# Optimization experiments

Measured on AMD Instinct MI355X. Metric: run time of the kernel, lower is better.

The kernel has to match this reference:

```python
import jax, jax.numpy as jnp
import numpy as np

N_NODES = 50000


def _gcn_norm(edge_index, num_nodes):
    # Add self-loops (PyG GCNConv default) and compute symmetric norm.
    loops = jnp.arange(num_nodes, dtype=edge_index.dtype)
    src = jnp.concatenate([edge_index[0], loops])
    dst = jnp.concatenate([edge_index[1], loops])
    ones = jnp.ones(src.shape[0], dtype=jnp.float32)
    deg = jax.ops.segment_sum(ones, dst, num_segments=num_nodes)
    deg_inv_sqrt = jnp.where(deg > 0, jax.lax.rsqrt(jnp.maximum(deg, 1.0)), 0.0)
    norm = deg_inv_sqrt[src] * deg_inv_sqrt[dst]  # [E + N]
    return src, dst, norm


def _gcn_conv(x, src, dst, norm, W, b, num_nodes):
    xw = x @ W                               # [N, out]
    msg = xw[src] * norm[:, None]            # gather + scale  [E+N, out]
    out = jax.ops.segment_sum(msg, dst, num_segments=num_nodes)  # scatter-add
    return out + b


def setup_inputs() -> dict:
    key = jax.random.key(0)
    ks = jax.random.split(key, 10)
    d_in, d_h, d_out = 64, 64, 8
    n_edges = 800000
    x = jax.random.normal(ks[0], (N_NODES, d_in), dtype=jnp.float32)
    edge_index = jax.random.randint(ks[1], (2, n_edges), 0, N_NODES, dtype=jnp.int64)
    def w(k, fan_in, fan_out):
        return jax.random.normal(k, (fan_in, fan_out), dtype=jnp.float32) * (1.0 / np.sqrt(fan_in))
    return {
        "x": x,
        "edge_index": edge_index,
        "W0": w(ks[2], d_in, d_h), "b0": jnp.zeros((d_h,), jnp.float32),
        "W1": w(ks[3], d_h, d_h), "b1": jnp.zeros((d_h,), jnp.float32),
        "W2": w(ks[4], d_h, d_h), "b2": jnp.zeros((d_h,), jnp.float32),
        "linW": w(ks[5], d_h, d_out), "linb": jnp.zeros((d_out,), jnp.float32),
    }


def reference(x, edge_index, W0, b0, W1, b1, W2, b2, linW, linb):
    num_nodes = x.shape[0]
    src, dst, norm = _gcn_norm(edge_index, num_nodes)
    # 3 GCNConv layers, ReLU; dropout is identity at inference (training=False).
    for W, b in ((W0, b0), (W1, b1), (W2, b2)):
        x = jax.nn.relu(_gcn_conv(x, src, dst, norm, W, b, num_nodes))
    return x @ linW + linb
```

## Files before the change

kernel.cpp:

```cpp
#include <hip/hip_runtime.h>
#include <hip/hip_fp16.h>

#define TPB 256
#define CAP 16384
#define CAPSH 14
#define SC_BLOCKS 256
#define MAXE 16

typedef __attribute__((ext_vector_type(8))) float f32x8;
typedef __attribute__((ext_vector_type(8))) unsigned short u16x8;


__device__ __forceinline__ int ld_idx(const void* p, long long i, int is64) {
    return is64 ? (int)((const long long*)p)[i] : ((const int*)p)[i];
}

__device__ __forceinline__ ushort4 f4_to_h4(float4 v) {
    ushort4 r;
    r.x = __half_as_ushort(__float2half_rn(v.x));
    r.y = __half_as_ushort(__float2half_rn(v.y));
    r.z = __half_as_ushort(__float2half_rn(v.z));
    r.w = __half_as_ushort(__float2half_rn(v.w));
    return r;
}

__global__ __launch_bounds__(TPB) void p3_scatter(const void* ei, long long E,
                                                  int* gcur, int* pairs) {
    __shared__ int cnt[TPB];
    __shared__ int cur2[TPB];
    __shared__ int s_is64;
    int t = threadIdx.x;
    if (t < 64) {
        const unsigned int* w = (const unsigned int*)ei;
        unsigned long long m = __ballot(w[2 * t + 1] != 0u);
        if (t == 0) s_is64 = (m == 0ull) ? 1 : 0;
    }
    cnt[t] = 0;
    __syncthreads();
    const int is64 = s_is64;
    long long chunk = (E + SC_BLOCKS - 1) / SC_BLOCKS;
    long long s0 = (long long)blockIdx.x * chunk;
    long long s1 = (s0 + chunk < E) ? s0 + chunk : E;

    int pk[MAXE];
    int bk[MAXE];
    int ne = 0;
    #pragma unroll
    for (int i = 0; i < MAXE; ++i) {
        long long e = s0 + t + (long long)i * TPB;
        if (e < s1) {
            int sv = ld_idx(ei, e, is64);
            int d  = ld_idx(ei, E + e, is64);
            pk[i] = (sv << 8) | (d & 255);
            bk[i] = d >> 8;
            atomicAdd(&cnt[bk[i]], 1);
            ne++;
        }
    }
    __syncthreads();
    if (cnt[t]) cur2[t] = (t << CAPSH) + atomicAdd(&gcur[t], cnt[t]);
    __syncthreads();
    #pragma unroll
    for (int i = 0; i < MAXE; ++i) {
        if (i < ne) {
            int pos = atomicAdd(&cur2[bk[i]], 1);
            pairs[pos] = pk[i];
        }
    }
}

__global__ __launch_bounds__(TPB) void p4_fill(const int* __restrict__ pairs,
                                               const int* __restrict__ gcur,
                                               const float* __restrict__ x,
                                               int2* __restrict__ meta,
                                               int* __restrict__ csr,
                                               ushort4* __restrict__ z0, int N) {
    __shared__ int ldeg[TPB];
    __shared__ int ssc[TPB];
    __shared__ int cur[TPB];
    __shared__ float fdis[TPB];
    int t = threadIdx.x;
    int b = blockIdx.x;
    int base = b << CAPSH;
    int ecnt = gcur[b];
    ldeg[t] = 0;
    __syncthreads();
    for (int e = base + t; e < base + ecnt; e += TPB)
        atomicAdd(&ldeg[pairs[e] & 255], 1);
    __syncthreads();
    int dv = ldeg[t];
    int pv = (dv + 7) & ~7;
    ssc[t] = pv;
    __syncthreads();
    for (int off = 1; off < TPB; off <<= 1) {
        int u = 0;
        if (t >= off) u = ssc[t - off];
        __syncthreads();
        ssc[t] += u;
        __syncthreads();
    }
    int o = base + ssc[t] - pv;
    cur[t] = o;
    float dd = rsqrtf((float)(dv + 1));
    fdis[t] = dd;
    int node = (b << 8) + t;
    if (node < N)
        meta[node] = make_int2((o << 8) | (pv >> 3), __float_as_int(dd));
    __syncthreads();
    for (int e = base + t; e < base + ecnt; e += TPB) {
        int p = pairs[e];
        int pos = atomicAdd(&cur[p & 255], 1);
        csr[pos] = p >> 8;
    }
    for (int e = o + dv; e < o + pv; ++e) csr[e] = N;

    int ni = t >> 4, c = t & 15;
    for (int p = 0; p < 16; ++p) {
        int nd = (b << 8) + p * 16 + ni;
        if (nd < N) {
            float dvv = fdis[p * 16 + ni];
            float4 h = ((const float4*)x)[(size_t)nd * 16 + c];
            float4 r = {h.x * dvv, h.y * dvv, h.z * dvv, h.w * dvv};
            z0[(size_t)nd * 16 + c] = f4_to_h4(r);
        }
    }
    if (b == 0 && t < 16) z0[(size_t)N * 16 + t] = make_ushort4(0, 0, 0, 0);
}

__device__ __forceinline__ f32x8 gather_rows(const u16x8* __restrict__ z8,
                                             const int* __restrict__ csr,
                                             int start, int nbatch, int c,
                                             f32x8 acc) {
    const int base = threadIdx.x & 56;
    int idx = (nbatch > 0) ? csr[start + c] : 0;
    for (int bt = 0; bt < nbatch; ++bt) {
        int nidx = (bt + 1 < nbatch) ? csr[start + (bt + 1) * 8 + c] : 0;
        #pragma unroll
        for (int k = 0; k < 8; ++k) {
            int s = __shfl(idx, base + k);
            u16x8 v = z8[(size_t)s * 8 + c];
            #pragma unroll
            for (int i = 0; i < 8; ++i)
                acc[i] += __half2float(__ushort_as_half(v[i]));
        }
        idx = nidx;
    }
    return acc;
}

__device__ __forceinline__ f32x8 shfl_mm8(f32x8 s, const float4* Ws4, int c) {
    const int base = threadIdx.x & 56;
    f32x8 u = {0.f, 0.f, 0.f, 0.f, 0.f, 0.f, 0.f, 0.f};
    #pragma unroll
    for (int q = 0; q < 8; ++q) {
        #pragma unroll
        for (int r = 0; r < 8; ++r) {
            float hv = __shfl(s[r], base + q);
            float4 w0 = Ws4[(q * 8 + r) * 16 + 2 * c];
            float4 w1 = Ws4[(q * 8 + r) * 16 + 2 * c + 1];
            u[0] = fmaf(hv, w0.x, u[0]);
            u[1] = fmaf(hv, w0.y, u[1]);
            u[2] = fmaf(hv, w0.z, u[2]);
            u[3] = fmaf(hv, w0.w, u[3]);
            u[4] = fmaf(hv, w1.x, u[4]);
            u[5] = fmaf(hv, w1.y, u[5]);
            u[6] = fmaf(hv, w1.z, u[6]);
            u[7] = fmaf(hv, w1.w, u[7]);
        }
    }
    return u;
}

__device__ __forceinline__ u16x8 f8_to_h8(f32x8 v) {
    u16x8 r;
    #pragma unroll
    for (int i = 0; i < 8; ++i)
        r[i] = __half_as_ushort(__float2half_rn(v[i]));
    return r;
}

__global__ __launch_bounds__(TPB) void layer_mm(const u16x8* __restrict__ z,
                                                const int* __restrict__ csr,
                                                const int2* __restrict__ meta,
                                                const float* __restrict__ b,
                                                const float* __restrict__ W,
                                                u16x8* __restrict__ zout, int n) {
    __shared__ float Ws[64 * 64];
    int t = threadIdx.x;
    float4* Ws4 = (float4*)Ws;
    const float4* W4g = (const float4*)W;
    #pragma unroll
    for (int i = 0; i < 4; ++i) Ws4[t + i * TPB] = W4g[t + i * TPB];

    if (blockIdx.x == 0 && t < 8) {
        u16x8 zz = {0, 0, 0, 0, 0, 0, 0, 0};
        zout[(size_t)n * 8 + t] = zz;
    }

    int wave = t >> 6, lane = t & 63;
    int g = lane >> 3, c = lane & 7;
    int node = blockIdx.x * 32 + wave * 8 + g;
    f32x8 s = {0.f, 0.f, 0.f, 0.f, 0.f, 0.f, 0.f, 0.f};
    float dv = 0.f;
    if (node < n) {
        int2 m = meta[node];
        int start = ((unsigned)m.x) >> 8;
        int nbatch = m.x & 255;
        dv = __int_as_float(m.y);
        u16x8 v = z[(size_t)node * 8 + c];
        #pragma unroll
        for (int i = 0; i < 8; ++i) s[i] = __half2float(__ushort_as_half(v[i]));
        s = gather_rows(z, csr, start, nbatch, c, s);
    }
    __syncthreads();
    f32x8 u = shfl_mm8(s, Ws4, c);
    if (node < n) {
        float4 b0 = ((const float4*)b)[2 * c];
        float4 b1 = ((const float4*)b)[2 * c + 1];
        f32x8 r;
        r[0] = fmaxf(fmaf(dv, u[0], b0.x), 0.f) * dv;
        r[1] = fmaxf(fmaf(dv, u[1], b0.y), 0.f) * dv;
        r[2] = fmaxf(fmaf(dv, u[2], b0.z), 0.f) * dv;
        r[3] = fmaxf(fmaf(dv, u[3], b0.w), 0.f) * dv;
        r[4] = fmaxf(fmaf(dv, u[4], b1.x), 0.f) * dv;
        r[5] = fmaxf(fmaf(dv, u[5], b1.y), 0.f) * dv;
        r[6] = fmaxf(fmaf(dv, u[6], b1.z), 0.f) * dv;
        r[7] = fmaxf(fmaf(dv, u[7], b1.w), 0.f) * dv;
        zout[(size_t)node * 8 + c] = f8_to_h8(r);
    }
}

__global__ __launch_bounds__(TPB) void layer_final(const u16x8* __restrict__ z,
                                                   const int* __restrict__ csr,
                                                   const int2* __restrict__ meta,
                                                   const float* __restrict__ b,
                                                   const float* __restrict__ W,
                                                   const float* __restrict__ Wl,
                                                   const float* __restrict__ bl,
                                                   float* __restrict__ out, int n) {
    __shared__ float Ws[64 * 64];
    __shared__ float Wls[64 * 8];
    __shared__ float bls[8];
    int t = threadIdx.x;
    float4* Ws4 = (float4*)Ws;
    const float4* W4g = (const float4*)W;
    #pragma unroll
    for (int i = 0; i < 4; ++i) Ws4[t + i * TPB] = W4g[t + i * TPB];
    if (t < 128) ((float4*)Wls)[t] = ((const float4*)Wl)[t];
    if (t < 8) bls[t] = bl[t];

    int wave = t >> 6, lane = t & 63;
    int g = lane >> 3, c = lane & 7;
    int node = blockIdx.x * 32 + wave * 8 + g;
    f32x8 s = {0.f, 0.f, 0.f, 0.f, 0.f, 0.f, 0.f, 0.f};
    float dv = 0.f;
    if (node < n) {
        int2 m = meta[node];
        int start = ((unsigned)m.x) >> 8;
        int nbatch = m.x & 255;
        dv = __int_as_float(m.y);
        u16x8 v = z[(size_t)node * 8 + c];
        #pragma unroll
        for (int i = 0; i < 8; ++i) s[i] = __half2float(__ushort_as_half(v[i]));
        s = gather_rows(z, csr, start, nbatch, c, s);
    }
    __syncthreads();
    f32x8 u = shfl_mm8(s, Ws4, c);
    float4 b0 = ((const float4*)b)[2 * c];
    float4 b1 = ((const float4*)b)[2 * c + 1];
    f32x8 h;
    h[0] = fmaxf(fmaf(dv, u[0], b0.x), 0.f);
    h[1] = fmaxf(fmaf(dv, u[1], b0.y), 0.f);
    h[2] = fmaxf(fmaf(dv, u[2], b0.z), 0.f);
    h[3] = fmaxf(fmaf(dv, u[3], b0.w), 0.f);
    h[4] = fmaxf(fmaf(dv, u[4], b1.x), 0.f);
    h[5] = fmaxf(fmaf(dv, u[5], b1.y), 0.f);
    h[6] = fmaxf(fmaf(dv, u[6], b1.z), 0.f);
    h[7] = fmaxf(fmaf(dv, u[7], b1.w), 0.f);

    const int base = threadIdx.x & 56;
    float acc = bls[c];
    #pragma unroll
    for (int q = 0; q < 8; ++q) {
        #pragma unroll
        for (int r = 0; r < 8; ++r) {
            float hv = __shfl(h[r], base + q);
            acc = fmaf(hv, Wls[(q * 8 + r) * 8 + c], acc);
        }
    }
    if (node < n) out[(size_t)node * 8 + c] = acc;
}

extern "C" void kernel_launch(void* const* d_in, const int* in_sizes, int n_in,
                              void* d_out, int out_size, void* d_ws, size_t ws_size,
                              hipStream_t stream) {
    const float* x  = (const float*)d_in[0];
    const void*  ei = d_in[1];
    const float* W0 = (const float*)d_in[2];
    const float* b0 = (const float*)d_in[3];
    const float* W1 = (const float*)d_in[4];
    const float* b1 = (const float*)d_in[5];
    const float* W2 = (const float*)d_in[6];
    const float* b2 = (const float*)d_in[7];
    const float* Wl = (const float*)d_in[8];
    const float* bl = (const float*)d_in[9];

    const long long E = in_sizes[1] / 2;
    const int dh = in_sizes[3];
    const int din = in_sizes[2] / dh;
    const int N = in_sizes[0] / din;
    const int nb = (N + 255) >> 8;

    char* ws = (char*)d_ws;
    size_t off = 0;
    auto alloc = [&](size_t bytes) -> char* {
        char* r = ws + off;
        off += (bytes + 255) & ~(size_t)255;
        return r;
    };
    int*   gcur    = (int*)  alloc(1024);
    int2*  meta    = (int2*) alloc((size_t)N * 8);
    int*   pairs   = (int*)  alloc((size_t)nb * CAP * 4);
    int*   csr     = (int*)  alloc((size_t)nb * CAP * 4);
    u16x8* zbA     = (u16x8*)alloc((size_t)(N + 1) * 64 * 2);
    u16x8* zbB     = (u16x8*)alloc((size_t)(N + 1) * 64 * 2);

    hipMemsetAsync(gcur, 0, 256 * sizeof(int), stream);
    p3_scatter<<<SC_BLOCKS, TPB, 0, stream>>>(ei, E, gcur, pairs);
    p4_fill<<<nb, TPB, 0, stream>>>(pairs, gcur, x, meta, csr,
                                    (ushort4*)zbA, N);

    const int gL = (N + 31) / 32;
    layer_mm<<<gL, TPB, 0, stream>>>(zbA, csr, meta, b0, W0, zbB, N);
    layer_mm<<<gL, TPB, 0, stream>>>(zbB, csr, meta, b1, W1, zbA, N);
    layer_final<<<gL, TPB, 0, stream>>>(zbA, csr, meta, b2, W2, Wl, bl,
                                        (float*)d_out, N);
}
```

Baseline: 186.7 us.

## Sort nodes by degree within each bucket to balance wavefront gather work

Adds a per-block counting sort of the 256 nodes in each bucket by in-degree, written to a perm array during CSR build. The layer kernels now read their node index through perm, so the 8 node groups sharing a wavefront have similar neighbour counts and less lane divergence in the gather loop. The cost is an extra histogram and scan in p4_fill, one extra indirect load per node, and less contiguous access to node rows in the layer kernels. Padding nodes (index >= N) are placed in the perm and skipped.

```diff
diff --git a/kernel.cpp b/kernel.cpp
--- a/kernel.cpp
+++ b/kernel.cpp
@@ -74,10 +74,12 @@
                                                const float* __restrict__ x,
                                                int2* __restrict__ meta,
                                                int* __restrict__ csr,
+                                               int* __restrict__ perm,
                                                ushort4* __restrict__ z0, int N) {
     __shared__ int ldeg[TPB];
     __shared__ int ssc[TPB];
     __shared__ int cur[TPB];
+    __shared__ int dh[TPB];
     __shared__ float fdis[TPB];
     int t = threadIdx.x;
     int b = blockIdx.x;
@@ -113,6 +115,26 @@
         csr[pos] = p >> 8;
     }
     for (int e = o + dv; e < o + pv; ++e) csr[e] = N;
+
+    int dkey = (node < N) ? ((dv > 255) ? 255 : dv) : 0;
+    dh[t] = 0;
+    __syncthreads();
+    atomicAdd(&dh[dkey], 1);
+    __syncthreads();
+    int hv = dh[t];
+    ssc[t] = hv;
+    __syncthreads();
+    for (int off = 1; off < TPB; off <<= 1) {
+        int u = 0;
+        if (t >= off) u = ssc[t - off];
+        __syncthreads();
+        ssc[t] += u;
+        __syncthreads();
+    }
+    dh[t] = ssc[t] - hv;
+    __syncthreads();
+    int rank = atomicAdd(&dh[dkey], 1);
+    perm[(b << 8) + rank] = node;
 
     int ni = t >> 4, c = t & 15;
     for (int p = 0; p < 16; ++p) {
@@ -182,6 +204,7 @@
 __global__ __launch_bounds__(TPB) void layer_mm(const u16x8* __restrict__ z,
                                                 const int* __restrict__ csr,
                                                 const int2* __restrict__ meta,
+                                                const int* __restrict__ perm,
                                                 const float* __restrict__ b,
                                                 const float* __restrict__ W,
                                                 u16x8* __restrict__ zout, int n) {
@@ -199,7 +222,7 @@
 
     int wave = t >> 6, lane = t & 63;
     int g = lane >> 3, c = lane & 7;
-    int node = blockIdx.x * 32 + wave * 8 + g;
+    int node = perm[blockIdx.x * 32 + wave * 8 + g];
     f32x8 s = {0.f, 0.f, 0.f, 0.f, 0.f, 0.f, 0.f, 0.f};
     float dv = 0.f;
     if (node < n) {
@@ -233,6 +256,7 @@
 __global__ __launch_bounds__(TPB) void layer_final(const u16x8* __restrict__ z,
                                                    const int* __restrict__ csr,
                                                    const int2* __restrict__ meta,
+                                                   const int* __restrict__ perm,
                                                    const float* __restrict__ b,
                                                    const float* __restrict__ W,
                                                    const float* __restrict__ Wl,
@@ -251,7 +275,7 @@
 
     int wave = t >> 6, lane = t & 63;
     int g = lane >> 3, c = lane & 7;
-    int node = blockIdx.x * 32 + wave * 8 + g;
+    int node = perm[blockIdx.x * 32 + wave * 8 + g];
     f32x8 s = {0.f, 0.f, 0.f, 0.f, 0.f, 0.f, 0.f, 0.f};
     float dv = 0.f;
     if (node < n) {
@@ -320,6 +344,7 @@
     };
     int*   gcur    = (int*)  alloc(1024);
     int2*  meta    = (int2*) alloc((size_t)N * 8);
+    int*   perm    = (int*)  alloc((size_t)nb * 256 * 4);
     int*   pairs   = (int*)  alloc((size_t)nb * CAP * 4);
     int*   csr     = (int*)  alloc((size_t)nb * CAP * 4);
     u16x8* zbA     = (u16x8*)alloc((size_t)(N + 1) * 64 * 2);
@@ -327,12 +352,12 @@
 
     hipMemsetAsync(gcur, 0, 256 * sizeof(int), stream);
     p3_scatter<<<SC_BLOCKS, TPB, 0, stream>>>(ei, E, gcur, pairs);
-    p4_fill<<<nb, TPB, 0, stream>>>(pairs, gcur, x, meta, csr,
+    p4_fill<<<nb, TPB, 0, stream>>>(pairs, gcur, x, meta, csr, perm,
                                     (ushort4*)zbA, N);
 
-    const int gL = (N + 31) / 32;
-    layer_mm<<<gL, TPB, 0, stream>>>(zbA, csr, meta, b0, W0, zbB, N);
-    layer_mm<<<gL, TPB, 0, stream>>>(zbB, csr, meta, b1, W1, zbA, N);
-    layer_final<<<gL, TPB, 0, stream>>>(zbA, csr, meta, b2, W2, Wl, bl,
+    const int gL = nb * 8;
+    layer_mm<<<gL, TPB, 0, stream>>>(zbA, csr, meta, perm, b0, W0, zbB, N);
+    layer_mm<<<gL, TPB, 0, stream>>>(zbB, csr, meta, perm, b1, W1, zbA, N);
+    layer_final<<<gL, TPB, 0, stream>>>(zbA, csr, meta, perm, b2, W2, Wl, bl,
                                         (float*)d_out, N);
 }
```

Measured after the change: 190.5 us. 2.1% more time.
